# Kernel tuning notes

Measured on AMD Instinct MI355X. Metric: run time of the kernel, lower is better.

The kernel has to match this reference:

```python
import jax, jax.numpy as jnp
import numpy as np

NHEAD = 4
NLAYERS = 4
C = 128
EPS = 1e-5


def ln(x, g, b):
    m = x.mean(-1, keepdims=True)
    v = jnp.var(x, axis=-1, keepdims=True)
    return (x - m) / jnp.sqrt(v + EPS) * g + b


def mha_rel(q_in, k_in, in_w, in_b, out_w, out_b, pos_enc, pos_idx, self_attn):
    # q_in/k_in: [W, N, C]; pos_enc: [2W-1, C]; pos_idx: [W*W] int
    w, bsz, c = q_in.shape
    hd = c // NHEAD
    scale = hd ** -0.5
    if self_attn:
        qkv = q_in @ in_w.T + in_b
        q, k, v = jnp.split(qkv, 3, axis=-1)
    else:
        q = q_in @ in_w[:c].T + in_b[:c]
        kv = k_in @ in_w[c:].T + in_b[c:]
        k, v = jnp.split(kv, 2, axis=-1)
    pe = pos_enc[pos_idx].reshape(w, w, c)             # [W, W', C] gathered rel-pos
    qr_kr = pe @ in_w[:2 * c].T + in_b[:2 * c]
    q_r, k_r = jnp.split(qr_kr, 2, axis=-1)
    q = (q * scale).reshape(w, bsz, NHEAD, hd)
    q_r = (q_r * scale).reshape(w, w, NHEAD, hd)
    k = k.reshape(w, bsz, NHEAD, hd)
    v = v.reshape(w, bsz, NHEAD, hd)
    k_r = k_r.reshape(w, w, NHEAD, hd)
    # content-content + content-pos + pos-content (STTR MultiheadAttentionRelative)
    attn = (jnp.einsum('wnec,vnec->newv', q, k)
            + jnp.einsum('wnec,wvec->newv', q, k_r)
            + jnp.einsum('vnec,wvec->newv', k, q_r))   # [N, E, W, W']
    raw = attn.sum(1)
    a = jax.nn.softmax(attn, axis=-1)
    v_o = jnp.einsum('newv,vnec->wnec', a, v).reshape(w, bsz, c)
    v_o = v_o @ out_w.T + out_b
    return v_o, a.sum(1) / NHEAD, raw


def _forward(feat_left, feat_right, pos_enc,
             s_iw, s_ib, s_ow, s_ob, s_g, s_b,
             c_iw, c_ib, c_ow, c_ob, c_g1, c_b1, c_g2, c_b2):
    bs, c, hn0, w = feat_left.shape
    hn = hn0 * bs

    def to_seq(x):  # [bs,c,hn,w] -> [w, hn*bs, c]
        return jnp.transpose(jnp.transpose(x, (1, 3, 2, 0)).reshape(c, w, hn), (1, 2, 0))

    fl = to_seq(feat_left)
    fr = to_seq(feat_right)
    pos_idx = (jnp.arange(w - 1, -1, -1)[:, None] + jnp.arange(w)[None, :]).reshape(-1)
    pos_flip = pos_enc[::-1]
    feat = jnp.concatenate([fl, fr], axis=1)           # [w, 2hn, c]
    for i in range(NLAYERS):
        # self attention over concatenated left/right
        f2 = ln(feat, s_g[i], s_b[i])
        f2, _, _ = mha_rel(f2, f2, s_iw[i], s_ib[i], s_ow[i], s_ob[i], pos_enc, pos_idx, True)
        feat = feat + f2
        # cross attention
        fl, fr = feat[:, :hn], feat[:, hn:]
        fl2 = ln(fl, c_g1[i], c_b1[i])
        fr2 = ln(fr, c_g1[i], c_b1[i])
        fr2u, _, _ = mha_rel(fr2, fl2, c_iw[i], c_ib[i], c_ow[i], c_ob[i], pos_flip, pos_idx, False)
        fr = fr + fr2u
        fr2n = ln(fr, c_g2[i], c_b2[i])
        fl2u, _, _ = mha_rel(fl2, fr2n, c_iw[i], c_ib[i], c_ow[i], c_ob[i], pos_enc, pos_idx, False)
        fl = fl + fl2u
        feat = jnp.concatenate([fl, fr], axis=1)
    return feat


def setup_inputs() -> dict:
    key = jax.random.key(0)
    ks = jax.random.split(key, 20)
    bs, hn, w = 2, 64, 192
    p = 0.02
    return {
        "feat_left": jax.random.normal(ks[0], (bs, C, hn, w), jnp.float32),
        "feat_right": jax.random.normal(ks[1], (bs, C, hn, w), jnp.float32),
        "pos_enc": jax.random.normal(ks[2], (2 * w - 1, C), jnp.float32),
        "s_iw": jax.random.normal(ks[3], (NLAYERS, 3 * C, C), jnp.float32) * p,
        "s_ib": jax.random.normal(ks[4], (NLAYERS, 3 * C), jnp.float32) * p,
        "s_ow": jax.random.normal(ks[5], (NLAYERS, C, C), jnp.float32) * p,
        "s_ob": jax.random.normal(ks[6], (NLAYERS, C), jnp.float32) * p,
        "s_g": jnp.ones((NLAYERS, C), jnp.float32),
        "s_b": jnp.zeros((NLAYERS, C), jnp.float32),
        "c_iw": jax.random.normal(ks[7], (NLAYERS, 3 * C, C), jnp.float32) * p,
        "c_ib": jax.random.normal(ks[8], (NLAYERS, 3 * C), jnp.float32) * p,
        "c_ow": jax.random.normal(ks[9], (NLAYERS, C, C), jnp.float32) * p,
        "c_ob": jax.random.normal(ks[10], (NLAYERS, C), jnp.float32) * p,
        "c_g1": jnp.ones((NLAYERS, C), jnp.float32),
        "c_b1": jnp.zeros((NLAYERS, C), jnp.float32),
        "c_g2": jnp.ones((NLAYERS, C), jnp.float32),
        "c_b2": jnp.zeros((NLAYERS, C), jnp.float32),
    }


def reference(feat_left, feat_right, pos_enc,
              s_iw, s_ib, s_ow, s_ob, s_g, s_b,
              c_iw, c_ib, c_ow, c_ob, c_g1, c_b1, c_g2, c_b2):
    return _forward(feat_left, feat_right, pos_enc,
                    s_iw, s_ib, s_ow, s_ob, s_g, s_b,
                    c_iw, c_ib, c_ow, c_ob, c_g1, c_b1, c_g2, c_b2)
```

## Files before the change

kernel.cpp:

```cpp
#include <hip/hip_runtime.h>
#include <hip/hip_bf16.h>
#include <math.h>

#define WW 192
#define NTOT 256
#define HNN 128
#define CC 128
#define NH 4
#define NLAY 4
#define EPSF 1e-5f
#define SCALE 0.17677669529663687f

typedef __attribute__((ext_vector_type(8))) short short8_t;
typedef __attribute__((ext_vector_type(4))) float f32x4;

#define MFMA(a, b, c) __builtin_amdgcn_mfma_f32_16x16x32_bf16(a, b, c, 0, 0, 0)

__device__ __forceinline__ ushort f2b(float f) {
  union { float f; uint u; } x; x.f = f;
  uint r = x.u + 0x7fffu + ((x.u >> 16) & 1u);
  return (ushort)(r >> 16);
}

__global__ __launch_bounds__(256) void k_build_feat(const float* __restrict__ L,
                                                    const float* __restrict__ R,
                                                    float* __restrict__ feat) {
  __shared__ float tile[32][33];
  int wt = blockIdx.x, h0 = blockIdx.y, z = blockIdx.z;
  int ct = z & 3, b = (z >> 2) & 1, side = z >> 3;
  const float* src = side ? R : L;
  int tx = threadIdx.x & 31, ty = threadIdx.x >> 5;
  const float* sp = src + ((size_t)(b * 128 + ct * 32) * 64 + h0) * 192 + wt * 32;
  #pragma unroll
  for (int yy = 0; yy < 4; ++yy) {
    int c = ty * 4 + yy;
    tile[c][tx] = sp[(size_t)c * 64 * 192 + tx];
  }
  __syncthreads();
  int n = 2 * h0 + b + side * 128;
  #pragma unroll
  for (int yy = 0; yy < 4; ++yy) {
    int w = ty * 4 + yy;
    feat[((size_t)(wt * 32 + w) * 256 + n) * 128 + ct * 32 + tx] = tile[tx][w];
  }
}

__global__ __launch_bounds__(256) void k_wconv(
    const float* __restrict__ s_iw, const float* __restrict__ s_ow,
    const float* __restrict__ c_iw, const float* __restrict__ c_ow,
    ushort* __restrict__ out) {
  int i4 = (blockIdx.x * 256 + threadIdx.x) * 4;
  const float* src;
  int off;
  if (i4 < 196608) { src = s_iw; off = i4; }
  else if (i4 < 262144) { src = s_ow; off = i4 - 196608; }
  else if (i4 < 458752) { src = c_iw; off = i4 - 262144; }
  else { src = c_ow; off = i4 - 458752; }
  float4 v = *(const float4*)(src + off);
  ushort4 o;
  o.x = f2b(v.x); o.y = f2b(v.y); o.z = f2b(v.z); o.w = f2b(v.w);
  *(ushort4*)(out + i4) = o;
}

__global__ __launch_bounds__(256) void k_ln(const float* __restrict__ src,
                                            ushort* __restrict__ dst,
                                            const float* __restrict__ g,
                                            const float* __restrict__ b,
                                            int n0, int nsub) {
  int t = blockIdx.x * 4 + (threadIdx.x >> 6);
  int lane = threadIdx.x & 63;
  int w = t / nsub, h = t - w * nsub;
  size_t row = (size_t)(w * NTOT + n0 + h) * CC;
  int c0 = lane * 2;
  float2 x = *(const float2*)(src + row + c0);
  float s = x.x + x.y;
  float s2 = x.x * x.x + x.y * x.y;
  #pragma unroll
  for (int o = 1; o < 64; o <<= 1) {
    s += __shfl_xor(s, o);
    s2 += __shfl_xor(s2, o);
  }
  float m = s * (1.0f / 128.0f);
  float var = s2 * (1.0f / 128.0f) - m * m;
  float inv = rsqrtf(var + EPSF);
  float oa = (x.x - m) * inv * g[c0] + b[c0];
  float ob = (x.y - m) * inv * g[c0 + 1] + b[c0 + 1];
  uint pack = (uint)f2b(oa) | ((uint)f2b(ob) << 16);
  *(uint*)(dst + row + c0) = pack;
}

__global__ __launch_bounds__(256) void k_gemm_bf16(
    const ushort* __restrict__ X, int xN, int x0,
    const ushort* __restrict__ Wb, const float* __restrict__ bias,
    ushort* __restrict__ Y, int yN, int y0, int ystride,
    int T, int nsub) {
  extern __shared__ char smem[];
  ushort* As = (ushort*)smem;
  ushort* Bs = As + 128 * 128;
  float* biasS = (float*)(Bs + 128 * 128);

  int bm = blockIdx.x, bn = blockIdx.y;
  int tid = threadIdx.x;

  {
    int row = tid >> 1;
    int ce0 = (tid & 1) * 64;
    int t = bm * 128 + row;
    int w = t / nsub, h = t - w * nsub;
    const ushort* src = X + (size_t)(w * xN + x0 + h) * CC + ce0;
    #pragma unroll
    for (int i = 0; i < 8; ++i) {
      short8_t v = *(const short8_t*)(src + i * 8);
      int cb = (ce0 + i * 8) * 2;
      *(short8_t*)((char*)As + row * 256 + (cb ^ ((row & 7) << 4))) = v;
    }
    const ushort* wsrc = Wb + (size_t)(bn * 128 + row) * CC + ce0;
    #pragma unroll
    for (int i = 0; i < 8; ++i) {
      short8_t v = *(const short8_t*)(wsrc + i * 8);
      int cb = (ce0 + i * 8) * 2;
      *(short8_t*)((char*)Bs + row * 256 + (cb ^ ((row & 7) << 4))) = v;
    }
    if (tid < 128) biasS[tid] = bias[bn * 128 + tid];
  }
  __syncthreads();

  int lane = tid & 63, wid = tid >> 6;
  int wm = (wid >> 1) * 64, wn = (wid & 1) * 64;
  int r = lane & 15, g = lane >> 4;

  f32x4 acc[4][4] = {};
  #pragma unroll
  for (int kc = 0; kc < 4; ++kc) {
    short8_t af[4], bf[4];
    #pragma unroll
    for (int mt = 0; mt < 4; ++mt) {
      int row = wm + mt * 16 + r;
      af[mt] = *(const short8_t*)((const char*)As + row * 256 + ((kc * 64 + g * 16) ^ ((row & 7) << 4)));
    }
    #pragma unroll
    for (int nt = 0; nt < 4; ++nt) {
      int row = wn + nt * 16 + r;
      bf[nt] = *(const short8_t*)((const char*)Bs + row * 256 + ((kc * 64 + g * 16) ^ ((row & 7) << 4)));
    }
    __builtin_amdgcn_s_setprio(1);
    #pragma unroll
    for (int mt = 0; mt < 4; ++mt)
      #pragma unroll
      for (int nt = 0; nt < 4; ++nt)
        acc[mt][nt] = MFMA(af[mt], bf[nt], acc[mt][nt]);
    __builtin_amdgcn_s_setprio(0);
  }

  #pragma unroll
  for (int mt = 0; mt < 4; ++mt) {
    #pragma unroll
    for (int reg = 0; reg < 4; ++reg) {
      int t = bm * 128 + wm + mt * 16 + g * 4 + reg;
      int w = t / nsub, h = t - w * nsub;
      size_t ybase = (size_t)(w * yN + y0 + h) * ystride + bn * 128;
      #pragma unroll
      for (int nt = 0; nt < 4; ++nt) {
        int nn = wn + nt * 16 + r;
        Y[ybase + nn] = f2b(acc[mt][nt][reg] + biasS[nn]);
      }
    }
  }
}

__global__ __launch_bounds__(256) void k_gemm_out(
    const ushort* __restrict__ X, int xN,
    const ushort* __restrict__ Wb, const float* __restrict__ bias,
    float* __restrict__ Y, int y0, float* __restrict__ Ymir,
    const float* __restrict__ g1, const float* __restrict__ b1,
    ushort* __restrict__ dst1, int d1N, int d1n0,
    const float* __restrict__ g2, const float* __restrict__ b2,
    ushort* __restrict__ dst2, int d2N, int d2n0,
    int T, int nsub) {
  extern __shared__ char smem[];
  ushort* As = (ushort*)smem;
  ushort* Bs = As + 128 * 128;
  float* biasS = (float*)(Bs + 128 * 128);
  float* rsum = biasS + 128;
  float* rsq  = rsum + 256;

  int bm = blockIdx.x;
  int tid = threadIdx.x;

  {
    int row = tid >> 1;
    int ce0 = (tid & 1) * 64;
    int t = bm * 128 + row;
    int w = t / nsub, h = t - w * nsub;
    const ushort* src = X + (size_t)(w * xN + h) * CC + ce0;
    #pragma unroll
    for (int i = 0; i < 8; ++i) {
      short8_t v = *(const short8_t*)(src + i * 8);
      int cb = (ce0 + i * 8) * 2;
      *(short8_t*)((char*)As + row * 256 + (cb ^ ((row & 7) << 4))) = v;
    }
    const ushort* wsrc = Wb + (size_t)row * CC + ce0;
    #pragma unroll
    for (int i = 0; i < 8; ++i) {
      short8_t v = *(const short8_t*)(wsrc + i * 8);
      int cb = (ce0 + i * 8) * 2;
      *(short8_t*)((char*)Bs + row * 256 + (cb ^ ((row & 7) << 4))) = v;
    }
    if (tid < 128) biasS[tid] = bias[tid];
  }
  __syncthreads();

  int lane = tid & 63, wid = tid >> 6;
  int wm = (wid >> 1) * 64, wn = (wid & 1) * 64;
  int r = lane & 15, g = lane >> 4;
  int g4 = g * 4;

  f32x4 acc[4][4] = {};
  #pragma unroll
  for (int kc = 0; kc < 4; ++kc) {
    short8_t af[4], bf[4];
    #pragma unroll
    for (int mt = 0; mt < 4; ++mt) {
      int row = wm + mt * 16 + r;
      af[mt] = *(const short8_t*)((const char*)As + row * 256 + ((kc * 64 + g * 16) ^ ((row & 7) << 4)));
    }
    #pragma unroll
    for (int nt = 0; nt < 4; ++nt) {
      int row = wn + nt * 16 + r;
      bf[nt] = *(const short8_t*)((const char*)Bs + row * 256 + ((kc * 64 + g * 16) ^ ((row & 7) << 4)));
    }
    __builtin_amdgcn_s_setprio(1);
    #pragma unroll
    for (int mt = 0; mt < 4; ++mt)
      #pragma unroll
      for (int nt = 0; nt < 4; ++nt)
        acc[mt][nt] = MFMA(af[mt], bf[nt], acc[mt][nt]);
    __builtin_amdgcn_s_setprio(0);
  }

  float nvv[4][4][4];
  #pragma unroll
  for (int mt = 0; mt < 4; ++mt) {
    #pragma unroll
    for (int reg = 0; reg < 4; ++reg) {
      int rloc = wm + mt * 16 + g4 + reg;
      int t = bm * 128 + rloc;
      int w = t / nsub, h = t - w * nsub;
      size_t ybase = (size_t)(w * NTOT + y0 + h) * CC;
      float s = 0.f, q = 0.f;
      #pragma unroll
      for (int nt = 0; nt < 4; ++nt) {
        int nn = wn + nt * 16 + r;
        float nv = Y[ybase + nn] + acc[mt][nt][reg] + biasS[nn];
        Y[ybase + nn] = nv;
        if (Ymir) Ymir[ybase + nn] = nv;
        nvv[mt][reg][nt] = nv;
        s += nv;
        q += nv * nv;
      }
      #pragma unroll
      for (int o = 1; o < 16; o <<= 1) {
        s += __shfl_xor(s, o);
        q += __shfl_xor(q, o);
      }
      if (r == 0) {
        rsum[rloc * 2 + (wn >> 6)] = s;
        rsq[rloc * 2 + (wn >> 6)] = q;
      }
    }
  }
  if (!dst1) return;
  __syncthreads();

  float g1c[4], b1c[4], g2c[4], b2c[4];
  #pragma unroll
  for (int nt = 0; nt < 4; ++nt) {
    int nn = wn + nt * 16 + r;
    g1c[nt] = g1[nn]; b1c[nt] = b1[nn];
    if (dst2) { g2c[nt] = g2[nn]; b2c[nt] = b2[nn]; }
  }
  #pragma unroll
  for (int mt = 0; mt < 4; ++mt) {
    #pragma unroll
    for (int reg = 0; reg < 4; ++reg) {
      int rloc = wm + mt * 16 + g4 + reg;
      int t = bm * 128 + rloc;
      int w = t / nsub, h = t - w * nsub;
      float S = rsum[rloc * 2] + rsum[rloc * 2 + 1];
      float Q = rsq[rloc * 2] + rsq[rloc * 2 + 1];
      float m = S * (1.0f / 128.0f);
      float inv = rsqrtf(Q * (1.0f / 128.0f) - m * m + EPSF);
      size_t d1base = (size_t)(w * d1N + d1n0 + h) * CC;
      size_t d2base = dst2 ? (size_t)(w * d2N + d2n0 + h) * CC : 0;
      #pragma unroll
      for (int nt = 0; nt < 4; ++nt) {
        int nn = wn + nt * 16 + r;
        float xn = (nvv[mt][reg][nt] - m) * inv;
        dst1[d1base + nn] = f2b(xn * g1c[nt] + b1c[nt]);
        if (dst2) dst2[d2base + nn] = f2b(xn * g2c[nt] + b2c[nt]);
      }
    }
  }
}

__global__ __launch_bounds__(256) void k_rr(
    const float* __restrict__ pos_enc,
    const float* __restrict__ s_iw, const float* __restrict__ s_ib,
    const float* __restrict__ c_iw, const float* __restrict__ c_ib,
    ushort* __restrict__ out_all) {
  extern __shared__ char smem[];
  ushort* As = (ushort*)smem;
  ushort* Bs = As + 128 * 128;
  float* biasS = (float*)(Bs + 128 * 128);

  int bm = blockIdx.x, bn = blockIdx.y, z = blockIdx.z;
  int layer = z >> 1;
  const float* Wt = ((z & 1) ? c_iw : s_iw) + (size_t)layer * 384 * CC;
  const float* bias = ((z & 1) ? c_ib : s_ib) + layer * 384;
  ushort* out = out_all + (size_t)z * 383 * 256;
  int tid = threadIdx.x;

  {
    int row = tid >> 1;
    int ce0 = (tid & 1) * 64;
    int t = bm * 128 + row;
    bool ok = (t < 383);
    const float* src = pos_enc + (size_t)t * CC + ce0;
    #pragma unroll
    for (int i = 0; i < 8; ++i) {
      float4 v0 = ok ? *(const float4*)(src + i * 8) : make_float4(0.f, 0.f, 0.f, 0.f);
      float4 v1 = ok ? *(const float4*)(src + i * 8 + 4) : make_float4(0.f, 0.f, 0.f, 0.f);
      short8_t pv;
      pv[0] = (short)f2b(v0.x); pv[1] = (short)f2b(v0.y);
      pv[2] = (short)f2b(v0.z); pv[3] = (short)f2b(v0.w);
      pv[4] = (short)f2b(v1.x); pv[5] = (short)f2b(v1.y);
      pv[6] = (short)f2b(v1.z); pv[7] = (short)f2b(v1.w);
      int cb = (ce0 + i * 8) * 2;
      *(short8_t*)((char*)As + row * 256 + (cb ^ ((row & 7) << 4))) = pv;
    }
    const float* wsrc = Wt + (size_t)(bn * 128 + row) * CC + ce0;
    #pragma unroll
    for (int i = 0; i < 8; ++i) {
      float4 v0 = *(const float4*)(wsrc + i * 8);
      float4 v1 = *(const float4*)(wsrc + i * 8 + 4);
      short8_t pv;
      pv[0] = (short)f2b(v0.x); pv[1] = (short)f2b(v0.y);
      pv[2] = (short)f2b(v0.z); pv[3] = (short)f2b(v0.w);
      pv[4] = (short)f2b(v1.x); pv[5] = (short)f2b(v1.y);
      pv[6] = (short)f2b(v1.z); pv[7] = (short)f2b(v1.w);
      int cb = (ce0 + i * 8) * 2;
      *(short8_t*)((char*)Bs + row * 256 + (cb ^ ((row & 7) << 4))) = pv;
    }
    if (tid < 128) biasS[tid] = bias[bn * 128 + tid];
  }
  __syncthreads();

  int lane = tid & 63, wid = tid >> 6;
  int wm = (wid >> 1) * 64, wn = (wid & 1) * 64;
  int r = lane & 15, g = lane >> 4;

  f32x4 acc[4][4] = {};
  #pragma unroll
  for (int kc = 0; kc < 4; ++kc) {
    short8_t af[4], bf[4];
    #pragma unroll
    for (int mt = 0; mt < 4; ++mt) {
      int row = wm + mt * 16 + r;
      af[mt] = *(const short8_t*)((const char*)As + row * 256 + ((kc * 64 + g * 16) ^ ((row & 7) << 4)));
    }
    #pragma unroll
    for (int nt = 0; nt < 4; ++nt) {
      int row = wn + nt * 16 + r;
      bf[nt] = *(const short8_t*)((const char*)Bs + row * 256 + ((kc * 64 + g * 16) ^ ((row & 7) << 4)));
    }
    #pragma unroll
    for (int mt = 0; mt < 4; ++mt)
      #pragma unroll
      for (int nt = 0; nt < 4; ++nt)
        acc[mt][nt] = MFMA(af[mt], bf[nt], acc[mt][nt]);
  }

  #pragma unroll
  for (int mt = 0; mt < 4; ++mt) {
    #pragma unroll
    for (int reg = 0; reg < 4; ++reg) {
      int t = bm * 128 + wm + mt * 16 + g * 4 + reg;
      if (t < 383) {
        #pragma unroll
        for (int nt = 0; nt < 4; ++nt) {
          int nn = wn + nt * 16 + r;
          out[(size_t)t * 256 + bn * 128 + nn] = f2b(acc[mt][nt][reg] + biasS[nn]);
        }
      }
    }
  }
}

#define KS_ST 36
#define VT_ST 196
#define B2_ST 37
#define PL_ST 20

template <int SGN>
__global__ __launch_bounds__(256, 4) void k_attn_mfma(
    const ushort* __restrict__ qbuf, int qstride, int qoff, int qN, int qn0,
    const ushort* __restrict__ kvbuf, int kvstride, int koff, int voff, int kN, int kn0,
    const ushort* __restrict__ rrb,
    ushort* __restrict__ obuf, int oN,
    int nblk) {
  __shared__ ushort Ks[192 * KS_ST];
  __shared__ ushort Vt[32 * VT_ST];
  __shared__ float Sb[4 * 16 * B2_ST];
  __shared__ uint PLb[4 * 16 * PL_ST];

  int bid = blockIdx.x;
  int n = bid % nblk;
  int rest = bid / nblk;
  int h = rest & 3;
  int ts = rest >> 2;
  int tid = threadIdx.x;
  int lane = tid & 63, wid = tid >> 6;
  int r = lane & 15, g = lane >> 4;
  int g4 = g * 4;

  for (int i = tid; i < 768; i += 256) {
    int row = i >> 2, c8 = (i & 3) * 8;
    *(short8_t*)&Ks[row * KS_ST + c8] =
        *(const short8_t*)(kvbuf + (size_t)(row * kN + kn0 + n) * kvstride + koff + h * 32 + c8);
  }
  {
    uint* Vtu = (uint*)Vt;
    for (int i = tid; i < 384; i += 256) {
      int dg = i / 96;
      int p = i - dg * 96;
      const ushort* vb = kvbuf + (size_t)((2 * p) * kN + kn0 + n) * kvstride + voff + h * 32 + dg * 8;
      short8_t a = *(const short8_t*)vb;
      short8_t b = *(const short8_t*)(vb + (size_t)kN * kvstride);
      #pragma unroll
      for (int j = 0; j < 8; ++j)
        Vtu[(dg * 8 + j) * 98 + p] = ((uint)(ushort)a[j]) | (((uint)(ushort)b[j]) << 16);
    }
  }
  int w0 = (ts * 4 + wid) * 16;
  short8_t qf = *(const short8_t*)(qbuf + (size_t)((w0 + r) * qN + qn0 + n) * qstride + qoff + h * 32 + g * 8);
  __syncthreads();

  float* flat = Sb + wid * 16 * B2_ST;
  uint* PL = PLb + wid * 16 * PL_ST;
  const ushort* KRg = rrb + 128 + h * 32 + g * 8;
  const ushort* QRg = rrb + h * 32 + g * 8;
  const f32x4 zf = {0.f, 0.f, 0.f, 0.f};

  int ca = (SGN < 0) ? (r + 1) : (31 - r);
  int cbn = (SGN < 0) ? (17 + r) : (15 - r);
  int rdcol = 16 - r + g4;

  f32x4 esum = zf, o0 = zf, o1 = zf;

  #pragma unroll
  for (int vp = 0; vp < 6; ++vp) {
    #pragma unroll
    for (int half = 0; half < 2; ++half) {
      int s = 2 * vp + half;
      int v0 = s * 16;
      short8_t kf = *(const short8_t*)&Ks[(v0 + r) * KS_ST + g * 8];
      int base2 = 176 + SGN * (w0 - v0);
      const ushort* krp = KRg + (size_t)(base2 + r) * 256;
      const ushort* qrp = QRg + (size_t)(base2 + r) * 256;
      short8_t krf0 = *(const short8_t*)krp;
      short8_t krf1 = *(const short8_t*)(krp + 16 * 256);
      short8_t qrf0 = *(const short8_t*)qrp;
      short8_t qrf1 = *(const short8_t*)(qrp + 16 * 256);
      __builtin_amdgcn_s_setprio(1);
      f32x4 t1  = MFMA(kf, qf, zf);
      f32x4 t3a = MFMA(kf, qrf0, zf);
      f32x4 t3b = MFMA(kf, qrf1, zf);
      f32x4 t2a = MFMA(qf, krf0, zf);
      f32x4 t2b = MFMA(qf, krf1, zf);
      __builtin_amdgcn_s_setprio(0);
      #pragma unroll
      for (int reg = 0; reg < 4; ++reg) {
        flat[(g4 + reg) * B2_ST + ca] = t2a[reg];
        flat[(g4 + reg) * B2_ST + cbn] = t2b[reg];
      }
      f32x4 p2v = *(const f32x4*)&flat[r * B2_ST + rdcol];
      f32x4 ev;
      #pragma unroll
      for (int reg = 0; reg < 4; ++reg) {
        int js = 15 + SGN * (r - g4 - reg);
        int idx = (lane & 48) | (js & 15);
        float v3a = __shfl(t3a[reg], idx);
        float v3b = __shfl(t3b[reg], idx);
        float p3 = (js < 16) ? v3a : v3b;
        float e = __expf((t1[reg] + p2v[reg] + p3) * SCALE);
        ev[reg] = e;
        esum[reg] += e;
      }
      uint pa = (uint)f2b(ev[0]) | ((uint)f2b(ev[1]) << 16);
      uint pbu = (uint)f2b(ev[2]) | ((uint)f2b(ev[3]) << 16);
      *(uint2*)&PL[r * PL_ST + 8 * half + 2 * g] = make_uint2(pa, pbu);
    }
    union { uint u[4]; short8_t s8; } pb;
    uint4 pr = *(const uint4*)&PL[r * PL_ST + 4 * g];
    pb.u[0] = pr.x; pb.u[1] = pr.y; pb.u[2] = pr.z; pb.u[3] = pr.w;
    short8_t vt0 = *(const short8_t*)&Vt[r * VT_ST + vp * 32 + g * 8];
    short8_t vt1 = *(const short8_t*)&Vt[(16 + r) * VT_ST + vp * 32 + g * 8];
    __builtin_amdgcn_s_setprio(1);
    o0 = MFMA(vt0, pb.s8, o0);
    o1 = MFMA(vt1, pb.s8, o1);
    __builtin_amdgcn_s_setprio(0);
  }

  float ssum = (esum[0] + esum[1]) + (esum[2] + esum[3]);
  ssum += __shfl_xor(ssum, 16);
  ssum += __shfl_xor(ssum, 32);

  float inv = 1.0f / ssum;
  ushort4 u0, u1;
  u0.x = f2b(o0[0] * inv); u0.y = f2b(o0[1] * inv);
  u0.z = f2b(o0[2] * inv); u0.w = f2b(o0[3] * inv);
  u1.x = f2b(o1[0] * inv); u1.y = f2b(o1[1] * inv);
  u1.z = f2b(o1[2] * inv); u1.w = f2b(o1[3] * inv);
  size_t rowb = (size_t)((w0 + r) * oN + n) * CC + h * 32;
  *(ushort4*)(obuf + rowb + g4) = u0;
  *(ushort4*)(obuf + rowb + 16 + g4) = u1;
}

extern "C" void kernel_launch(void* const* d_in, const int* in_sizes, int n_in,
                              void* d_out, int out_size, void* d_ws, size_t ws_size,
                              hipStream_t stream) {
  const float* feat_left  = (const float*)d_in[0];
  const float* feat_right = (const float*)d_in[1];
  const float* pos_enc    = (const float*)d_in[2];
  const float* s_iw = (const float*)d_in[3];
  const float* s_ib = (const float*)d_in[4];
  const float* s_ow = (const float*)d_in[5];
  const float* s_ob = (const float*)d_in[6];
  const float* s_g  = (const float*)d_in[7];
  const float* s_b  = (const float*)d_in[8];
  const float* c_iw = (const float*)d_in[9];
  const float* c_ib = (const float*)d_in[10];
  const float* c_ow = (const float*)d_in[11];
  const float* c_ob = (const float*)d_in[12];
  const float* c_g1 = (const float*)d_in[13];
  const float* c_b1 = (const float*)d_in[14];
  const float* c_g2 = (const float*)d_in[15];
  const float* c_b2 = (const float*)d_in[16];

  char* W = (char*)d_ws;
  float*  feat    = (float*)W;
  ushort* f2s     = (ushort*)(W + 25165824);
  ushort* qkv     = (ushort*)(W + 37748736);
  ushort* obuf    = (ushort*)(W + 75497472);
  ushort* kv2     = (ushort*)(W + 88080384);
  ushort* rrb_all = (ushort*)(W + 100663296);
  ushort* wbf     = (ushort*)(W + 102232064);

  ushort* f2c1 = f2s;
  ushort* f2c2 = obuf + WW * HNN * CC;

  const int GEMM_LDS = 128 * 128 * 2 * 2 + 128 * 4;
  const int OUT_LDS  = 128 * 128 * 2 * 2 + 128 * 4 + 2048;
  hipFuncSetAttribute(reinterpret_cast<const void*>(&k_gemm_bf16),
                      hipFuncAttributeMaxDynamicSharedMemorySize, GEMM_LDS);
  hipFuncSetAttribute(reinterpret_cast<const void*>(&k_gemm_out),
                      hipFuncAttributeMaxDynamicSharedMemorySize, OUT_LDS);
  hipFuncSetAttribute(reinterpret_cast<const void*>(&k_rr),
                      hipFuncAttributeMaxDynamicSharedMemorySize, GEMM_LDS);

  k_build_feat<<<dim3(6, 64, 16), 256, 0, stream>>>(feat_left, feat_right, feat);
  k_rr<<<dim3(3, 2, 8), 256, GEMM_LDS, stream>>>(pos_enc, s_iw, s_ib, c_iw, c_ib, rrb_all);
  k_wconv<<<512, 256, 0, stream>>>(s_iw, s_ow, c_iw, c_ow, wbf);

  const ushort* siw_bf_base = wbf;
  const ushort* sow_bf_base = wbf + 196608;
  const ushort* ciw_bf_base = wbf + 262144;
  const ushort* cow_bf_base = wbf + 458752;

  const int T_FULL = WW * NTOT;
  const int T_HALF = WW * HNN;

  k_ln<<<T_FULL / 4, 256, 0, stream>>>(feat, f2s, s_g, s_b, 0, NTOT);

  for (int i = 0; i < NLAY; ++i) {
    const float* sib = s_ib + i * 384;
    const float* sob = s_ob + i * CC;
    const float* cib = c_ib + i * 384;
    const float* cob = c_ob + i * CC;
    const ushort* siw_bf = siw_bf_base + (size_t)i * 384 * CC;
    const ushort* sow_bf = sow_bf_base + (size_t)i * CC * CC;
    const ushort* ciw_bf = ciw_bf_base + (size_t)i * 384 * CC;
    const ushort* cow_bf = cow_bf_base + (size_t)i * CC * CC;
    const ushort* rr_self  = rrb_all + (size_t)(2 * i) * 383 * 256;
    const ushort* rr_cross = rrb_all + (size_t)(2 * i + 1) * 383 * 256;
    int last = (i == NLAY - 1);
    float* mir = last ? (float*)d_out : nullptr;
    const float* sg_n = s_g + (i + 1) * CC;
    const float* sb_n = s_b + (i + 1) * CC;

    k_gemm_bf16<<<dim3(T_FULL / 128, 3), 256, GEMM_LDS, stream>>>(
        f2s, NTOT, 0, siw_bf, sib, qkv, NTOT, 0, 384, T_FULL, NTOT);
    k_attn_mfma<-1><<<NTOT * NH * 3, 256, 0, stream>>>(
        qkv, 384, 0, NTOT, 0, qkv, 384, 128, 256, NTOT, 0,
        rr_self, obuf, NTOT, NTOT);
    k_gemm_out<<<T_FULL / 128, 256, OUT_LDS, stream>>>(
        obuf, NTOT, sow_bf, sob, feat, 0, nullptr,
        c_g1 + i * CC, c_b1 + i * CC, f2c1, NTOT, 0,
        nullptr, nullptr, nullptr, 0, 0, T_FULL, NTOT);
    k_gemm_bf16<<<dim3(T_FULL / 128, 3), 256, GEMM_LDS, stream>>>(
        f2c1, NTOT, 0, ciw_bf, cib, qkv, NTOT, 0, 384, T_FULL, NTOT);
    k_attn_mfma<+1><<<HNN * NH * 3, 256, 0, stream>>>(
        qkv, 384, 0, NTOT, 128, qkv, 384, 128, 256, NTOT, 0,
        rr_cross, obuf, HNN, HNN);
    k_gemm_out<<<T_HALF / 128, 256, OUT_LDS, stream>>>(
        obuf, HNN, cow_bf, cob, feat, 128, mir,
        c_g2 + i * CC, c_b2 + i * CC, f2c2, HNN, 0,
        last ? nullptr : sg_n, sb_n, last ? nullptr : f2s, NTOT, 128,
        T_HALF, HNN);
    k_gemm_bf16<<<dim3(T_HALF / 128, 2), 256, GEMM_LDS, stream>>>(
        f2c2, HNN, 0, ciw_bf + 128 * CC, cib + 128, kv2, HNN, 0, 256, T_HALF, HNN);
    k_attn_mfma<-1><<<HNN * NH * 3, 256, 0, stream>>>(
        qkv, 384, 0, NTOT, 0, kv2, 256, 0, 128, HNN, 0,
        rr_cross, obuf, HNN, HNN);
    k_gemm_out<<<T_HALF / 128, 256, OUT_LDS, stream>>>(
        obuf, HNN, cow_bf, cob, feat, 0, mir,
        last ? nullptr : sg_n, sb_n, last ? nullptr : f2s, NTOT, 0,
        nullptr, nullptr, nullptr, 0, 0, T_HALF, HNN);
  }
}
```

Measured before the change: 1.208 ms.

## Fuse output projection, residual LayerNorm and next QKV projection GEMM

Adds a k_gemm_fused kernel that computes the attention output projection, adds the residual, applies LayerNorm, keeps the normalized tile in shared memory, and immediately runs the following input projection (QKV or KV) for that row tile. Two separate GEMM launches per layer go away, along with the global write and re-read of the normalized activations. In exchange, each block loops serially over the 2-3 output column tiles, so the grid has fewer blocks and less parallelism than the old 2D launch.

After: 1.258 ms. 1.04x slower.

```diff
diff --git a/kernel.cpp b/kernel.cpp
--- a/kernel.cpp
+++ b/kernel.cpp
@@ -174,8 +174,6 @@
     float* __restrict__ Y, int y0, float* __restrict__ Ymir,
     const float* __restrict__ g1, const float* __restrict__ b1,
     ushort* __restrict__ dst1, int d1N, int d1n0,
-    const float* __restrict__ g2, const float* __restrict__ b2,
-    ushort* __restrict__ dst2, int d2N, int d2n0,
     int T, int nsub) {
   extern __shared__ char smem[];
   ushort* As = (ushort*)smem;
@@ -272,12 +270,11 @@
   if (!dst1) return;
   __syncthreads();
 
-  float g1c[4], b1c[4], g2c[4], b2c[4];
+  float g1c[4], b1c[4];
   #pragma unroll
   for (int nt = 0; nt < 4; ++nt) {
     int nn = wn + nt * 16 + r;
     g1c[nt] = g1[nn]; b1c[nt] = b1[nn];
-    if (dst2) { g2c[nt] = g2[nn]; b2c[nt] = b2[nn]; }
   }
   #pragma unroll
   for (int mt = 0; mt < 4; ++mt) {
@@ -291,13 +288,201 @@
       float m = S * (1.0f / 128.0f);
       float inv = rsqrtf(Q * (1.0f / 128.0f) - m * m + EPSF);
       size_t d1base = (size_t)(w * d1N + d1n0 + h) * CC;
-      size_t d2base = dst2 ? (size_t)(w * d2N + d2n0 + h) * CC : 0;
       #pragma unroll
       for (int nt = 0; nt < 4; ++nt) {
         int nn = wn + nt * 16 + r;
         float xn = (nvv[mt][reg][nt] - m) * inv;
         dst1[d1base + nn] = f2b(xn * g1c[nt] + b1c[nt]);
-        if (dst2) dst2[d2base + nn] = f2b(xn * g2c[nt] + b2c[nt]);
+      }
+    }
+  }
+}
+
+__global__ __launch_bounds__(256) void k_gemm_fused(
+    const ushort* __restrict__ X, int xN,
+    const ushort* __restrict__ W1, const float* __restrict__ bias1,
+    float* __restrict__ Y, int y0, float* __restrict__ Ymir,
+    const float* __restrict__ gA, const float* __restrict__ bA,
+    const float* __restrict__ g2, const float* __restrict__ b2,
+    ushort* __restrict__ dst2, int d2N, int d2n0,
+    const ushort* __restrict__ W2, const float* __restrict__ bias2, int nbn2,
+    ushort* __restrict__ Y2, int y2N, int y2n0, int y2stride,
+    int T, int nsub) {
+  extern __shared__ char smem[];
+  ushort* As = (ushort*)smem;
+  ushort* Bs = As + 128 * 128;
+  float* biasS = (float*)(Bs + 128 * 128);
+  float* rsum = biasS + 128;
+  float* rsq  = rsum + 256;
+
+  int bm = blockIdx.x;
+  int tid = threadIdx.x;
+  int srow = tid >> 1;
+  int sce0 = (tid & 1) * 64;
+
+  {
+    int t = bm * 128 + srow;
+    int w = t / nsub, h = t - w * nsub;
+    const ushort* src = X + (size_t)(w * xN + h) * CC + sce0;
+    #pragma unroll
+    for (int i = 0; i < 8; ++i) {
+      short8_t v = *(const short8_t*)(src + i * 8);
+      int cb = (sce0 + i * 8) * 2;
+      *(short8_t*)((char*)As + srow * 256 + (cb ^ ((srow & 7) << 4))) = v;
+    }
+    const ushort* wsrc = W1 + (size_t)srow * CC + sce0;
+    #pragma unroll
+    for (int i = 0; i < 8; ++i) {
+      short8_t v = *(const short8_t*)(wsrc + i * 8);
+      int cb = (sce0 + i * 8) * 2;
+      *(short8_t*)((char*)Bs + srow * 256 + (cb ^ ((srow & 7) << 4))) = v;
+    }
+    if (tid < 128) biasS[tid] = bias1[tid];
+  }
+  __syncthreads();
+
+  int lane = tid & 63, wid = tid >> 6;
+  int wm = (wid >> 1) * 64, wn = (wid & 1) * 64;
+  int r = lane & 15, g = lane >> 4;
+  int g4 = g * 4;
+
+  f32x4 acc[4][4] = {};
+  #pragma unroll
+  for (int kc = 0; kc < 4; ++kc) {
+    short8_t af[4], bf[4];
+    #pragma unroll
+    for (int mt = 0; mt < 4; ++mt) {
+      int row = wm + mt * 16 + r;
+      af[mt] = *(const short8_t*)((const char*)As + row * 256 + ((kc * 64 + g * 16) ^ ((row & 7) << 4)));
+    }
+    #pragma unroll
+    for (int nt = 0; nt < 4; ++nt) {
+      int row = wn + nt * 16 + r;
+      bf[nt] = *(const short8_t*)((const char*)Bs + row * 256 + ((kc * 64 + g * 16) ^ ((row & 7) << 4)));
+    }
+    __builtin_amdgcn_s_setprio(1);
+    #pragma unroll
+    for (int mt = 0; mt < 4; ++mt)
+      #pragma unroll
+      for (int nt = 0; nt < 4; ++nt)
+        acc[mt][nt] = MFMA(af[mt], bf[nt], acc[mt][nt]);
+    __builtin_amdgcn_s_setprio(0);
+  }
+
+  float nvv[4][4][4];
+  #pragma unroll
+  for (int mt = 0; mt < 4; ++mt) {
+    #pragma unroll
+    for (int reg = 0; reg < 4; ++reg) {
+      int rloc = wm + mt * 16 + g4 + reg;
+      int t = bm * 128 + rloc;
+      int w = t / nsub, h = t - w * nsub;
+      size_t ybase = (size_t)(w * NTOT + y0 + h) * CC;
+      float s = 0.f, q = 0.f;
+      #pragma unroll
+      for (int nt = 0; nt < 4; ++nt) {
+        int nn = wn + nt * 16 + r;
+        float nv = Y[ybase + nn] + acc[mt][nt][reg] + biasS[nn];
+        Y[ybase + nn] = nv;
+        if (Ymir) Ymir[ybase + nn] = nv;
+        nvv[mt][reg][nt] = nv;
+        s += nv;
+        q += nv * nv;
+      }
+      #pragma unroll
+      for (int o = 1; o < 16; o <<= 1) {
+        s += __shfl_xor(s, o);
+        q += __shfl_xor(q, o);
+      }
+      if (r == 0) {
+        rsum[rloc * 2 + (wn >> 6)] = s;
+        rsq[rloc * 2 + (wn >> 6)] = q;
+      }
+    }
+  }
+  __syncthreads();
+
+  {
+    float gac[4], bac[4], g2c[4], b2c[4];
+    #pragma unroll
+    for (int nt = 0; nt < 4; ++nt) {
+      int nn = wn + nt * 16 + r;
+      gac[nt] = gA[nn]; bac[nt] = bA[nn];
+      if (dst2) { g2c[nt] = g2[nn]; b2c[nt] = b2[nn]; }
+    }
+    #pragma unroll
+    for (int mt = 0; mt < 4; ++mt) {
+      #pragma unroll
+      for (int reg = 0; reg < 4; ++reg) {
+        int rloc = wm + mt * 16 + g4 + reg;
+        int t = bm * 128 + rloc;
+        int w = t / nsub, h = t - w * nsub;
+        float S = rsum[rloc * 2] + rsum[rloc * 2 + 1];
+        float Q = rsq[rloc * 2] + rsq[rloc * 2 + 1];
+        float m = S * (1.0f / 128.0f);
+        float inv = rsqrtf(Q * (1.0f / 128.0f) - m * m + EPSF);
+        size_t d2base = dst2 ? (size_t)(w * d2N + d2n0 + h) * CC : 0;
+        #pragma unroll
+        for (int nt = 0; nt < 4; ++nt) {
+          int nn = wn + nt * 16 + r;
+          float xn = (nvv[mt][reg][nt] - m) * inv;
+          *(ushort*)((char*)As + rloc * 256 + ((nn * 2) ^ ((rloc & 7) << 4))) =
+              f2b(xn * gac[nt] + bac[nt]);
+          if (dst2) dst2[d2base + nn] = f2b(xn * g2c[nt] + b2c[nt]);
+        }
+      }
+    }
+  }
+
+  for (int bn2 = 0; bn2 < nbn2; ++bn2) {
+    __syncthreads();
+    {
+      const ushort* wsrc = W2 + (size_t)(bn2 * 128 + srow) * CC + sce0;
+      #pragma unroll
+      for (int i = 0; i < 8; ++i) {
+        short8_t v = *(const short8_t*)(wsrc + i * 8);
+        int cb = (sce0 + i * 8) * 2;
+        *(short8_t*)((char*)Bs + srow * 256 + (cb ^ ((srow & 7) << 4))) = v;
+      }
+      if (tid < 128) biasS[tid] = bias2[bn2 * 128 + tid];
+    }
+    __syncthreads();
+
+    f32x4 acc2[4][4] = {};
+    #pragma unroll
+    for (int kc = 0; kc < 4; ++kc) {
+      short8_t af[4], bf[4];
+      #pragma unroll
+      for (int mt = 0; mt < 4; ++mt) {
+        int row = wm + mt * 16 + r;
+        af[mt] = *(const short8_t*)((const char*)As + row * 256 + ((kc * 64 + g * 16) ^ ((row & 7) << 4)));
+      }
+      #pragma unroll
+      for (int nt = 0; nt < 4; ++nt) {
+        int row = wn + nt * 16 + r;
+        bf[nt] = *(const short8_t*)((const char*)Bs + row * 256 + ((kc * 64 + g * 16) ^ ((row & 7) << 4)));
+      }
+      __builtin_amdgcn_s_setprio(1);
+      #pragma unroll
+      for (int mt = 0; mt < 4; ++mt)
+        #pragma unroll
+        for (int nt = 0; nt < 4; ++nt)
+          acc2[mt][nt] = MFMA(af[mt], bf[nt], acc2[mt][nt]);
+      __builtin_amdgcn_s_setprio(0);
+    }
+
+    #pragma unroll
+    for (int mt = 0; mt < 4; ++mt) {
+      #pragma unroll
+      for (int reg = 0; reg < 4; ++reg) {
+        int t = bm * 128 + wm + mt * 16 + g4 + reg;
+        int w = t / nsub, h = t - w * nsub;
+        size_t ybase = (size_t)(w * y2N + y2n0 + h) * y2stride + bn2 * 128;
+        #pragma unroll
+        for (int nt = 0; nt < 4; ++nt) {
+          int nn = wn + nt * 16 + r;
+          Y2[ybase + nn] = f2b(acc2[mt][nt][reg] + biasS[nn]);
+        }
       }
     }
   }
@@ -556,14 +741,13 @@
   ushort* rrb_all = (ushort*)(W + 100663296);
   ushort* wbf     = (ushort*)(W + 102232064);
 
-  ushort* f2c1 = f2s;
-  ushort* f2c2 = obuf + WW * HNN * CC;
-
   const int GEMM_LDS = 128 * 128 * 2 * 2 + 128 * 4;
   const int OUT_LDS  = 128 * 128 * 2 * 2 + 128 * 4 + 2048;
   hipFuncSetAttribute(reinterpret_cast<const void*>(&k_gemm_bf16),
                       hipFuncAttributeMaxDynamicSharedMemorySize, GEMM_LDS);
   hipFuncSetAttribute(reinterpret_cast<const void*>(&k_gemm_out),
+                      hipFuncAttributeMaxDynamicSharedMemorySize, OUT_LDS);
+  hipFuncSetAttribute(reinterpret_cast<const void*>(&k_gemm_fused),
                       hipFuncAttributeMaxDynamicSharedMemorySize, OUT_LDS);
   hipFuncSetAttribute(reinterpret_cast<const void*>(&k_rr),
                       hipFuncAttributeMaxDynamicSharedMemorySize, GEMM_LDS);
@@ -603,28 +787,27 @@
     k_attn_mfma<-1><<<NTOT * NH * 3, 256, 0, stream>>>(
         qkv, 384, 0, NTOT, 0, qkv, 384, 128, 256, NTOT, 0,
         rr_self, obuf, NTOT, NTOT);
-    k_gemm_out<<<T_FULL / 128, 256, OUT_LDS, stream>>>(
+    k_gemm_fused<<<T_FULL / 128, 256, OUT_LDS, stream>>>(
         obuf, NTOT, sow_bf, sob, feat, 0, nullptr,
-        c_g1 + i * CC, c_b1 + i * CC, f2c1, NTOT, 0,
-        nullptr, nullptr, nullptr, 0, 0, T_FULL, NTOT);
-    k_gemm_bf16<<<dim3(T_FULL / 128, 3), 256, GEMM_LDS, stream>>>(
-        f2c1, NTOT, 0, ciw_bf, cib, qkv, NTOT, 0, 384, T_FULL, NTOT);
+        c_g1 + i * CC, c_b1 + i * CC,
+        nullptr, nullptr, nullptr, 0, 0,
+        ciw_bf, cib, 3, qkv, NTOT, 0, 384,
+        T_FULL, NTOT);
     k_attn_mfma<+1><<<HNN * NH * 3, 256, 0, stream>>>(
         qkv, 384, 0, NTOT, 128, qkv, 384, 128, 256, NTOT, 0,
         rr_cross, obuf, HNN, HNN);
-    k_gemm_out<<<T_HALF / 128, 256, OUT_LDS, stream>>>(
+    k_gemm_fused<<<T_HALF / 128, 256, OUT_LDS, stream>>>(
         obuf, HNN, cow_bf, cob, feat, 128, mir,
-        c_g2 + i * CC, c_b2 + i * CC, f2c2, HNN, 0,
+        c_g2 + i * CC, c_b2 + i * CC,
         last ? nullptr : sg_n, sb_n, last ? nullptr : f2s, NTOT, 128,
+        ciw_bf + 128 * CC, cib + 128, 2, kv2, HNN, 0, 256,
         T_HALF, HNN);
-    k_gemm_bf16<<<dim3(T_HALF / 128, 2), 256, GEMM_LDS, stream>>>(
-        f2c2, HNN, 0, ciw_bf + 128 * CC, cib + 128, kv2, HNN, 0, 256, T_HALF, HNN);
     k_attn_mfma<-1><<<HNN * NH * 3, 256, 0, stream>>>(
         qkv, 384, 0, NTOT, 0, kv2, 256, 0, 128, HNN, 0,
         rr_cross, obuf, HNN, HNN);
     k_gemm_out<<<T_HALF / 128, 256, OUT_LDS, stream>>>(
         obuf, HNN, cow_bf, cob, feat, 0, mir,
         last ? nullptr : sg_n, sb_n, last ? nullptr : f2s, NTOT, 0,
-        nullptr, nullptr, nullptr, 0, 0, T_HALF, HNN);
-  }
-}
+        T_HALF, HNN);
+  }
+}
```
